# Performance work log

Hardware: AMD Instinct MI355X
Metric: run time of the kernel (lower is better)

Reference implementation:

```python
import jax, jax.numpy as jnp
import numpy as np

EPS = 1e-5
KEY_DIM = 32
V_DIM = 128  # att_ratio * key_dim
HEADS = 8


def bn2d(x, g, b):
    # BatchNorm2d, training-mode batch statistics: per-channel over (B, H, W)
    m = x.mean(axis=(0, 2, 3), keepdims=True)
    v = x.var(axis=(0, 2, 3), keepdims=True)
    xh = (x - m) * jax.lax.rsqrt(v + EPS)
    return xh * g[None, :, None, None] + b[None, :, None, None]


def conv1x1(x, w):
    # [B,Cin,H,W] x [Cout,Cin] -> [B,Cout,H,W]
    return jnp.einsum('bchw,oc->bohw', x, w)


def setup_inputs() -> dict:
    key = jax.random.key(0)
    ks = jax.random.split(key, 6)
    B, C, H, W = 8, 384, 32, 32
    s = 0.02
    return {
        'x': jax.random.normal(ks[0], (B, C, H, W), jnp.float32),
        'w_qkv': jax.random.normal(ks[1], (1536, 384), jnp.float32) * s,
        'g_qkv': jnp.ones((1536,), jnp.float32),
        'b_qkv': jnp.zeros((1536,), jnp.float32),
        'w_merge': jax.random.normal(ks[2], (384, 1024), jnp.float32) * s,
        'g_merge': jnp.ones((384,), jnp.float32),
        'b_merge': jnp.zeros((384,), jnp.float32),
        'w_fc1': jax.random.normal(ks[3], (768, 384), jnp.float32) * s,
        'g_fc1': jnp.ones((768,), jnp.float32),
        'b_fc1': jnp.zeros((768,), jnp.float32),
        'w_fc2': jax.random.normal(ks[4], (384, 768), jnp.float32) * s,
        'g_fc2': jnp.ones((384,), jnp.float32),
        'b_fc2': jnp.zeros((384,), jnp.float32),
    }


def reference(x, w_qkv, g_qkv, b_qkv, w_merge, g_merge, b_merge,
              w_fc1, g_fc1, b_fc1, w_fc2, g_fc2, b_fc2):
    B, C, H, W = x.shape
    N = H * W
    scale = KEY_DIM ** -0.5

    # ---- Attention block (conv path) ----
    qkv = bn2d(conv1x1(x, w_qkv), g_qkv, b_qkv)            # [B,1536,H,W]
    qkv = qkv.reshape(B, HEADS, KEY_DIM + KEY_DIM + V_DIM, N)
    q = qkv[:, :, :KEY_DIM]                                 # [B,h,dq,N]
    k = qkv[:, :, KEY_DIM:2 * KEY_DIM]                      # [B,h,dk,N]
    v = qkv[:, :, 2 * KEY_DIM:]                             # [B,h,dv,N]
    att = jnp.einsum('bhdn,bhdm->bhnm', q, k) * scale       # [B,h,N,N]
    att = jax.nn.softmax(att, axis=-1)
    o = jnp.einsum('bhnm,bhdm->bhdn', att, v)               # [B,h,dv,N]
    o = o.reshape(B, HEADS * V_DIM, H, W)                   # [B,1024,H,W]
    o = jax.nn.gelu(o, approximate=False)                   # merge.act
    o = bn2d(conv1x1(o, w_merge), g_merge, b_merge)         # [B,384,H,W]
    x = x + o                                               # residual

    # ---- ConvMlp block ----
    h = bn2d(conv1x1(x, w_fc1), g_fc1, b_fc1)               # [B,768,H,W]
    h = jax.nn.gelu(h, approximate=False)
    h = bn2d(conv1x1(h, w_fc2), g_fc2, b_fc2)               # [B,384,H,W]
    return x + h
```

## Files before the change

### kernel.cpp

```cpp
#include <hip/hip_runtime.h>
#include <hip/hip_bf16.h>
#include <math.h>


#define NPIX 1024
typedef __attribute__((ext_vector_type(8))) short short8;
typedef __attribute__((ext_vector_type(4))) float f32x4;
typedef unsigned long long ull;

__device__ __forceinline__ float gelu_exact(float v) {
    return 0.5f * v * (1.0f + erff(v * 0.70710678118654752f));
}
__device__ __forceinline__ short f2bf(float f) {
    unsigned u = __float_as_uint(f);
    unsigned r = (u + 0x7fffu + ((u >> 16) & 1u)) >> 16;
    return (short)r;
}
__device__ __forceinline__ ull pack4bf(float a, float b, float c, float d) {
    return  (ull)(unsigned short)f2bf(a)
         | ((ull)(unsigned short)f2bf(b) << 16)
         | ((ull)(unsigned short)f2bf(c) << 32)
         | ((ull)(unsigned short)f2bf(d) << 48);
}

__global__ __launch_bounds__(256) void cast4(
    const float* __restrict__ s0, const float* __restrict__ s1,
    const float* __restrict__ s2, const float* __restrict__ s3,
    short* __restrict__ d0, short* __restrict__ d1,
    short* __restrict__ d2, short* __restrict__ d3)
{
    int t = blockIdx.x * 256 + threadIdx.x;
    const float* s; short* d; int off;
    if (t < 73728)       { s = s0; d = d0; off = t; }
    else if (t < 122880) { s = s1; d = d1; off = t - 73728; }
    else if (t < 159744) { s = s2; d = d2; off = t - 122880; }
    else                 { s = s3; d = d3; off = t - 159744; }
    float4 a = *(const float4*)&s[(size_t)off * 8];
    float4 b = *(const float4*)&s[(size_t)off * 8 + 4];
    *(ull*)&d[(size_t)off * 8]     = pack4bf(a.x, a.y, a.z, a.w);
    *(ull*)&d[(size_t)off * 8 + 4] = pack4bf(b.x, b.y, b.z, b.w);
}

__global__ __launch_bounds__(256) void x_transpose(
    const float* __restrict__ x, short* __restrict__ x_bf, float* __restrict__ x_tf)
{
    __shared__ float ls[64][65];
    const int b = blockIdx.z, c0 = blockIdx.y * 64, n0 = blockIdx.x * 64;
    const int rl = threadIdx.x >> 6, ll = threadIdx.x & 63;
    #pragma unroll
    for (int it = 0; it < 16; ++it) {
        int c = rl + it * 4;
        ls[c][ll] = x[((size_t)b * 384 + c0 + c) * NPIX + n0 + ll];
    }
    __syncthreads();
    #pragma unroll
    for (int it = 0; it < 16; ++it) {
        int n = rl + it * 4;
        float v = ls[ll][n];
        size_t row = (size_t)b * NPIX + n0 + n;
        x_tf[row * 384 + c0 + ll] = v;
        x_bf[row * 384 + c0 + ll] = f2bf(v);
    }
}

__global__ __launch_bounds__(256) void gemm_bf16(
    const short* __restrict__ A, const short* __restrict__ Wt,
    float* __restrict__ D, float* __restrict__ sums, int O, int K)
{
    __shared__ short a_s[128 * 72];
    __shared__ short w_s[128 * 72];
    const int tid = threadIdx.x;
    const int wave = tid >> 6, lane = tid & 63;
    const int l16 = lane & 15, lhi = lane >> 4;
    const int m0 = blockIdx.x * 128, o0 = blockIdx.y * 128;
    const int wm = (wave & 1) * 64, wo = (wave >> 1) * 64;

    f32x4 acc[4][4];
    #pragma unroll
    for (int i = 0; i < 4; ++i)
        #pragma unroll
        for (int j = 0; j < 4; ++j) acc[i][j] = (f32x4){0.f, 0.f, 0.f, 0.f};

    for (int k0 = 0; k0 < K; k0 += 64) {
        #pragma unroll
        for (int it = 0; it < 4; ++it) {
            int idx = tid + it * 256;
            int r = idx >> 3, ch = idx & 7;
            *(float4*)&a_s[r * 72 + ch * 8] =
                *(const float4*)&A[(size_t)(m0 + r) * K + k0 + ch * 8];
            *(float4*)&w_s[r * 72 + ch * 8] =
                *(const float4*)&Wt[(size_t)(o0 + r) * K + k0 + ch * 8];
        }
        __syncthreads();
        #pragma unroll
        for (int kb = 0; kb < 2; ++kb) {
            short8 af[4], wf[4];
            #pragma unroll
            for (int i = 0; i < 4; ++i)
                af[i] = *(const short8*)&a_s[(wm + i * 16 + l16) * 72 + kb * 32 + lhi * 8];
            #pragma unroll
            for (int j = 0; j < 4; ++j)
                wf[j] = *(const short8*)&w_s[(wo + j * 16 + l16) * 72 + kb * 32 + lhi * 8];
            #pragma unroll
            for (int i = 0; i < 4; ++i)
                #pragma unroll
                for (int j = 0; j < 4; ++j)
                    acc[i][j] = __builtin_amdgcn_mfma_f32_16x16x32_bf16(af[i], wf[j], acc[i][j], 0, 0, 0);
        }
        __syncthreads();
    }

    #pragma unroll
    for (int i = 0; i < 4; ++i) {
        #pragma unroll
        for (int r = 0; r < 4; ++r) {
            size_t row = (size_t)(m0 + wm + i * 16 + lhi * 4 + r);
            #pragma unroll
            for (int j = 0; j < 4; ++j)
                D[row * O + o0 + wo + j * 16 + l16] = acc[i][j][r];
        }
    }
    #pragma unroll
    for (int j = 0; j < 4; ++j) {
        float s1 = 0.f, s2 = 0.f;
        #pragma unroll
        for (int i = 0; i < 4; ++i)
            #pragma unroll
            for (int r = 0; r < 4; ++r) { float v = acc[i][j][r]; s1 += v; s2 += v * v; }
        s1 += __shfl_xor(s1, 16); s1 += __shfl_xor(s1, 32);
        s2 += __shfl_xor(s2, 16); s2 += __shfl_xor(s2, 32);
        if (lhi == 0) {
            int col = o0 + wo + j * 16 + l16;
            atomicAdd(&sums[col * 2], s1);
            atomicAdd(&sums[col * 2 + 1], s2);
        }
    }
}

__global__ __launch_bounds__(256) void bn_finalize(
    const float* __restrict__ sums, const float* __restrict__ gamma,
    const float* __restrict__ beta, float* __restrict__ st, int O)
{
    int ch = blockIdx.x * 256 + threadIdx.x;
    if (ch >= O) return;
    float s = sums[ch * 2], ss = sums[ch * 2 + 1];
    float mean = s * (1.0f / 8192.0f);
    float var = ss * (1.0f / 8192.0f) - mean * mean;
    float sc = gamma[ch] * rsqrtf(var + 1e-5f);
    st[ch * 2] = sc;
    st[ch * 2 + 1] = beta[ch] - mean * sc;
}

__global__ __launch_bounds__(256) void qkv_post_vt(
    const float* __restrict__ raw, const float* __restrict__ st,
    short* __restrict__ qko, short* __restrict__ vto)
{
    __shared__ short ls[64][136];
    const int b = blockIdx.z, hp = blockIdx.y, n0 = blockIdx.x * 64;
    const int tid = threadIdx.x;
    const int r = tid >> 2, cg = tid & 3;
    const size_t rowbase = (size_t)(b * NPIX + n0 + r) * 1536;
    const float qs = 0.17677669529663687f * 1.4426950408889634f;

    {
        int hh = 2 * hp + (cg >> 1);
        int chb = hh * 192 + (cg & 1) * 32;
        bool isq = (cg & 1) == 0;
        size_t orow = (size_t)(b * NPIX + n0 + r) * 512 + hp * 128 + cg * 32;
        #pragma unroll
        for (int cc = 0; cc < 8; ++cc) {
            int ch = chb + cc * 4;
            float4 v  = *(const float4*)&raw[rowbase + ch];
            float4 sa = *(const float4*)&st[ch * 2];
            float4 sb = *(const float4*)&st[ch * 2 + 4];
            float o0 = v.x * sa.x + sa.y, o1 = v.y * sa.z + sa.w;
            float o2 = v.z * sb.x + sb.y, o3 = v.w * sb.z + sb.w;
            if (isq) { o0 *= qs; o1 *= qs; o2 *= qs; o3 *= qs; }
            *(ull*)&qko[orow + cc * 4] = pack4bf(o0, o1, o2, o3);
        }
    }
    #pragma unroll
    for (int hv = 0; hv < 2; ++hv) {
        int h = 2 * hp + hv;
        __syncthreads();
        #pragma unroll
        for (int cc = 0; cc < 8; ++cc) {
            int ch = h * 192 + 64 + cg * 32 + cc * 4;
            float4 v  = *(const float4*)&raw[rowbase + ch];
            float4 sa = *(const float4*)&st[ch * 2];
            float4 sb = *(const float4*)&st[ch * 2 + 4];
            float o0 = v.x * sa.x + sa.y, o1 = v.y * sa.z + sa.w;
            float o2 = v.z * sb.x + sb.y, o3 = v.w * sb.z + sb.w;
            *(ull*)&ls[r][cg * 32 + cc * 4] = pack4bf(o0, o1, o2, o3);
        }
        __syncthreads();
        int dv = tid >> 1, nh = tid & 1;
        size_t obase = ((size_t)(b * 8 + h) * 128 + dv) * NPIX + n0 + nh * 32;
        #pragma unroll
        for (int j = 0; j < 8; ++j) {
            int n = nh * 32 + j * 4;
            ull u =  (ull)(unsigned short)ls[n][dv]
                  | ((ull)(unsigned short)ls[n + 1][dv] << 16)
                  | ((ull)(unsigned short)ls[n + 2][dv] << 32)
                  | ((ull)(unsigned short)ls[n + 3][dv] << 48);
            *(ull*)&vto[obase + j * 4] = u;
        }
    }
}

#define ATTN_TILE(M0, KCUR, KNEXT)                                            \
{                                                                             \
    const int m0_ = (M0);                                                     \
    f32x4 s0_[4], s1_[4];                                                     \
    _Pragma("unroll")                                                         \
    for (int fm = 0; fm < 4; ++fm) {                                          \
        s0_[fm] = (f32x4){0.f, 0.f, 0.f, 0.f};                                \
        s1_[fm] = (f32x4){0.f, 0.f, 0.f, 0.f};                                \
    }                                                                         \
    _Pragma("unroll")                                                         \
    for (int fm = 0; fm < 4; ++fm) {                                          \
        s0_[fm] = __builtin_amdgcn_mfma_f32_16x16x32_bf16(KCUR[fm], qf0, s0_[fm], 0, 0, 0); \
        s1_[fm] = __builtin_amdgcn_mfma_f32_16x16x32_bf16(KCUR[fm], qf1, s1_[fm], 0, 0, 0); \
    }                                                                         \
    short8 vf_[16];                                                           \
    _Pragma("unroll")                                                         \
    for (int kc = 0; kc < 2; ++kc)                                            \
        _Pragma("unroll")                                                     \
        for (int fdv = 0; fdv < 8; ++fdv)                                     \
            vf_[kc * 8 + fdv] = *(const short8*)&vb[(size_t)(fdv * 16 + l16) * NPIX + m0_ + kc * 32 + lhi * 8]; \
    {                                                                         \
        int mn_ = (m0_ + 64) & 1023;                                          \
        _Pragma("unroll")                                                     \
        for (int fm = 0; fm < 4; ++fm)                                        \
            KNEXT[fm] = *(const short8*)&kb[(size_t)(mn_ + fm * 16 + l16) * 512 + lhi * 8]; \
    }                                                                         \
    float mx0 = fmaxf(fmaxf(s0_[0][0], s0_[0][1]), fmaxf(s0_[0][2], s0_[0][3])); \
    float mx1 = fmaxf(fmaxf(s1_[0][0], s1_[0][1]), fmaxf(s1_[0][2], s1_[0][3])); \
    _Pragma("unroll")                                                         \
    for (int fm = 1; fm < 4; ++fm) {                                          \
        mx0 = fmaxf(mx0, fmaxf(fmaxf(s0_[fm][0], s0_[fm][1]), fmaxf(s0_[fm][2], s0_[fm][3]))); \
        mx1 = fmaxf(mx1, fmaxf(fmaxf(s1_[fm][0], s1_[fm][1]), fmaxf(s1_[fm][2], s1_[fm][3]))); \
    }                                                                         \
    mx0 = fmaxf(mx0, __shfl_xor(mx0, 16)); mx0 = fmaxf(mx0, __shfl_xor(mx0, 32)); \
    mx1 = fmaxf(mx1, __shfl_xor(mx1, 16)); mx1 = fmaxf(mx1, __shfl_xor(mx1, 32)); \
    bool need_ = (mx0 > m_run0 + 11.0f) || (mx1 > m_run1 + 11.0f);            \
    if (__any(need_)) {                                                       \
        float mn0 = fmaxf(m_run0, mx0), f0 = exp2f(m_run0 - mn0);             \
        float mn1 = fmaxf(m_run1, mx1), f1 = exp2f(m_run1 - mn1);             \
        m_run0 = mn0; m_run1 = mn1; l_run0 *= f0; l_run1 *= f1;               \
        _Pragma("unroll")                                                     \
        for (int rr = 0; rr < 4; ++rr) {                                      \
            float fb0 = __shfl(f0, lhi * 4 + rr);                             \
            float fb1 = __shfl(f1, lhi * 4 + rr);                             \
            _Pragma("unroll")                                                 \
            for (int fdv = 0; fdv < 8; ++fdv) {                               \
                acc[0][fdv][rr] *= fb0;                                       \
                acc[1][fdv][rr] *= fb1;                                       \
            }                                                                 \
        }                                                                     \
    }                                                                         \
    float rs0 = 0.f, rs1 = 0.f;                                               \
    _Pragma("unroll")                                                         \
    for (int fm = 0; fm < 4; ++fm) {                                          \
        float p0 = exp2f(s0_[fm][0] - m_run0), p1 = exp2f(s0_[fm][1] - m_run0); \
        float p2 = exp2f(s0_[fm][2] - m_run0), p3 = exp2f(s0_[fm][3] - m_run0); \
        rs0 += (p0 + p1) + (p2 + p3);                                         \
        *(ull*)&pw[l16 * 72 + fm * 16 + lhi * 4] = pack4bf(p0, p1, p2, p3);   \
        float t0 = exp2f(s1_[fm][0] - m_run1), t1 = exp2f(s1_[fm][1] - m_run1); \
        float t2 = exp2f(s1_[fm][2] - m_run1), t3 = exp2f(s1_[fm][3] - m_run1); \
        rs1 += (t0 + t1) + (t2 + t3);                                         \
        *(ull*)&pw[(16 + l16) * 72 + fm * 16 + lhi * 4] = pack4bf(t0, t1, t2, t3); \
    }                                                                         \
    rs0 += __shfl_xor(rs0, 16); rs0 += __shfl_xor(rs0, 32);                   \
    rs1 += __shfl_xor(rs1, 16); rs1 += __shfl_xor(rs1, 32);                   \
    l_run0 += rs0; l_run1 += rs1;                                             \
    asm volatile("s_waitcnt lgkmcnt(0)" ::: "memory");                        \
    _Pragma("unroll")                                                         \
    for (int kc = 0; kc < 2; ++kc) {                                          \
        short8 pf0 = *(const short8*)&pw[l16 * 72 + kc * 32 + lhi * 8];       \
        short8 pf1 = *(const short8*)&pw[(16 + l16) * 72 + kc * 32 + lhi * 8]; \
        _Pragma("unroll")                                                     \
        for (int fdv = 0; fdv < 8; ++fdv) {                                   \
            acc[0][fdv] = __builtin_amdgcn_mfma_f32_16x16x32_bf16(pf0, vf_[kc * 8 + fdv], acc[0][fdv], 0, 0, 0); \
            acc[1][fdv] = __builtin_amdgcn_mfma_f32_16x16x32_bf16(pf1, vf_[kc * 8 + fdv], acc[1][fdv], 0, 0, 0); \
        }                                                                     \
    }                                                                         \
}

__global__ __launch_bounds__(64) void attn_kernel(
    const short* __restrict__ qk, const short* __restrict__ vt, short* __restrict__ outp)
{
    __shared__ short pw[32 * 72];
    const int id0 = blockIdx.x;
    const int swz = (id0 & 7) * 256 + (id0 >> 3);
    const int qt = swz & 31, bh = swz >> 5;
    const int h = bh & 7, b = bh >> 3;
    const int q0 = qt * 32;
    const int lane = threadIdx.x;
    const int l16 = lane & 15, lhi = lane >> 4;

    const short* qkb = qk + (size_t)b * NPIX * 512 + h * 64;
    const short* kb  = qkb + 32;
    const short* vb  = vt + (size_t)bh * 128 * NPIX;

    short8 qf0 = *(const short8*)&qkb[(size_t)(q0 + l16) * 512 + lhi * 8];
    short8 qf1 = *(const short8*)&qkb[(size_t)(q0 + 16 + l16) * 512 + lhi * 8];

    f32x4 acc[2][8];
    #pragma unroll
    for (int i = 0; i < 2; ++i)
        #pragma unroll
        for (int j = 0; j < 8; ++j) acc[i][j] = (f32x4){0.f, 0.f, 0.f, 0.f};
    float m_run0 = -1e30f, m_run1 = -1e30f, l_run0 = 0.f, l_run1 = 0.f;

    short8 kfA[4], kfB[4];
    #pragma unroll
    for (int fm = 0; fm < 4; ++fm)
        kfA[fm] = *(const short8*)&kb[(size_t)(fm * 16 + l16) * 512 + lhi * 8];

    for (int mt = 0; mt < 16; mt += 2) {
        ATTN_TILE(mt * 64,      kfA, kfB)
        ATTN_TILE(mt * 64 + 64, kfB, kfA)
    }

    #pragma unroll
    for (int rr = 0; rr < 4; ++rr) {
        float inv0 = 1.0f / __shfl(l_run0, lhi * 4 + rr);
        float inv1 = 1.0f / __shfl(l_run1, lhi * 4 + rr);
        size_t row0 = (size_t)b * NPIX + q0 + lhi * 4 + rr;
        #pragma unroll
        for (int fdv = 0; fdv < 8; ++fdv) {
            float o0 = acc[0][fdv][rr] * inv0;
            float o1 = acc[1][fdv][rr] * inv1;
            outp[row0 * 1024 + h * 128 + fdv * 16 + l16] = f2bf(gelu_exact(o0));
            outp[(row0 + 16) * 1024 + h * 128 + fdv * 16 + l16] = f2bf(gelu_exact(o1));
        }
    }
}

__global__ __launch_bounds__(256) void x2_kernel(
    const float* __restrict__ raw, const float* __restrict__ st,
    const float* __restrict__ xtf, float* __restrict__ x2f, short* __restrict__ x2bf)
{
    int t = blockIdx.x * 256 + threadIdx.x;
    int row = t / 96, c = (t % 96) * 4;
    size_t idx = (size_t)row * 384 + c;
    float4 v  = *(const float4*)&raw[idx];
    float4 xr = *(const float4*)&xtf[idx];
    float4 sa = *(const float4*)&st[c * 2];
    float4 sb = *(const float4*)&st[c * 2 + 4];
    float o0 = xr.x + v.x * sa.x + sa.y;
    float o1 = xr.y + v.y * sa.z + sa.w;
    float o2 = xr.z + v.z * sb.x + sb.y;
    float o3 = xr.w + v.w * sb.z + sb.w;
    *(float4*)&x2f[idx] = make_float4(o0, o1, o2, o3);
    *(ull*)&x2bf[idx] = pack4bf(o0, o1, o2, o3);
}

__global__ __launch_bounds__(256) void h_kernel(
    const float* __restrict__ raw, const float* __restrict__ st, short* __restrict__ hbf)
{
    int t = blockIdx.x * 256 + threadIdx.x;
    int row = t / 192, c = (t % 192) * 4;
    size_t idx = (size_t)row * 768 + c;
    float4 v  = *(const float4*)&raw[idx];
    float4 sa = *(const float4*)&st[c * 2];
    float4 sb = *(const float4*)&st[c * 2 + 4];
    float o0 = gelu_exact(v.x * sa.x + sa.y);
    float o1 = gelu_exact(v.y * sa.z + sa.w);
    float o2 = gelu_exact(v.z * sb.x + sb.y);
    float o3 = gelu_exact(v.w * sb.z + sb.w);
    *(ull*)&hbf[idx] = pack4bf(o0, o1, o2, o3);
}

__global__ __launch_bounds__(256) void final_tr(
    const float* __restrict__ raw, const float* __restrict__ st,
    const float* __restrict__ x2f, float* __restrict__ out)
{
    __shared__ float ls[64][65];
    const int b = blockIdx.z, c0 = blockIdx.y * 64, n0 = blockIdx.x * 64;
    const int rl = threadIdx.x >> 6, ll = threadIdx.x & 63;
    const int c = c0 + ll;
    const float sc = st[c * 2], sh = st[c * 2 + 1];
    #pragma unroll
    for (int it = 0; it < 16; ++it) {
        int n = rl + it * 4;
        size_t idx = ((size_t)b * NPIX + n0 + n) * 384 + c;
        ls[n][ll] = x2f[idx] + raw[idx] * sc + sh;
    }
    __syncthreads();
    #pragma unroll
    for (int it = 0; it < 16; ++it) {
        int cr = rl + it * 4;
        out[((size_t)b * 384 + c0 + cr) * NPIX + n0 + ll] = ls[ll][cr];
    }
}

extern "C" void kernel_launch(void* const* d_in, const int* in_sizes, int n_in,
                              void* d_out, int out_size, void* d_ws, size_t ws_size,
                              hipStream_t stream)
{
    const float* x       = (const float*)d_in[0];
    const float* w_qkv   = (const float*)d_in[1];
    const float* g_qkv   = (const float*)d_in[2];
    const float* b_qkv   = (const float*)d_in[3];
    const float* w_merge = (const float*)d_in[4];
    const float* g_merge = (const float*)d_in[5];
    const float* b_merge = (const float*)d_in[6];
    const float* w_fc1   = (const float*)d_in[7];
    const float* g_fc1   = (const float*)d_in[8];
    const float* b_fc1   = (const float*)d_in[9];
    const float* w_fc2   = (const float*)d_in[10];
    const float* g_fc2   = (const float*)d_in[11];
    const float* b_fc2   = (const float*)d_in[12];
    float* out = (float*)d_out;

    char* ws = (char*)d_ws;
    short* wq_bf   = (short*)(ws + 0);
    short* wm_bf   = (short*)(ws + 1179648);
    short* wf1_bf  = (short*)(ws + 1966080);
    short* wf2_bf  = (short*)(ws + 2555904);
    short* x_bf    = (short*)(ws + 3145728);
    float* x_tf    = (float*)(ws + 9437184);
    float* qkv_raw = (float*)(ws + 22020096);
    short* qk_bf   = (short*)(ws + 72351744);
    short* vt      = (short*)(ws + 80740352);
    short* attn_bf = (short*)(ws + 22020096);
    float* fc1_raw = (float*)(ws + 38797312);
    float* fc2_raw = (float*)(ws + 22020096);
    short* h_bf    = (short*)(ws + 80740352);
    float* merge_raw = (float*)(ws + 97517568);
    short* x2_bf   = (short*)(ws + 110100480);
    float* x2_f    = (float*)(ws + 116391936);
    float* sums    = (float*)(ws + 128974848);
    float* stats   = (float*)(ws + 128999424);

    float* sums_qkv = sums;
    float* sums_mg  = sums + 1536 * 2;
    float* sums_f1  = sums + (1536 + 384) * 2;
    float* sums_f2  = sums + (1536 + 384 + 768) * 2;
    float* st_qkv = stats;
    float* st_mg  = stats + 1536 * 2;
    float* st_f1  = stats + (1536 + 384) * 2;
    float* st_f2  = stats + (1536 + 384 + 768) * 2;

    hipMemsetAsync(sums, 0, 3072 * 2 * sizeof(float), stream);

    cast4<<<768, 256, 0, stream>>>(w_qkv, w_merge, w_fc1, w_fc2,
                                   wq_bf, wm_bf, wf1_bf, wf2_bf);
    x_transpose<<<dim3(16, 6, 8), 256, 0, stream>>>(x, x_bf, x_tf);

    gemm_bf16<<<dim3(64, 12), 256, 0, stream>>>(x_bf, wq_bf, qkv_raw, sums_qkv, 1536, 384);
    bn_finalize<<<6, 256, 0, stream>>>(sums_qkv, g_qkv, b_qkv, st_qkv, 1536);
    qkv_post_vt<<<dim3(16, 4, 8), 256, 0, stream>>>(qkv_raw, st_qkv, qk_bf, vt);

    attn_kernel<<<2048, 64, 0, stream>>>(qk_bf, vt, attn_bf);

    gemm_bf16<<<dim3(64, 3), 256, 0, stream>>>(attn_bf, wm_bf, merge_raw, sums_mg, 384, 1024);
    bn_finalize<<<2, 256, 0, stream>>>(sums_mg, g_merge, b_merge, st_mg, 384);
    x2_kernel<<<3072, 256, 0, stream>>>(merge_raw, st_mg, x_tf, x2_f, x2_bf);

    gemm_bf16<<<dim3(64, 6), 256, 0, stream>>>(x2_bf, wf1_bf, fc1_raw, sums_f1, 768, 384);
    bn_finalize<<<3, 256, 0, stream>>>(sums_f1, g_fc1, b_fc1, st_f1, 768);
    h_kernel<<<6144, 256, 0, stream>>>(fc1_raw, sums_f1 == sums_f1 ? st_f1 : st_f1, h_bf);

    gemm_bf16<<<dim3(64, 3), 256, 0, stream>>>(h_bf, wf2_bf, fc2_raw, sums_f2, 384, 768);
    bn_finalize<<<2, 256, 0, stream>>>(sums_f2, g_fc2, b_fc2, st_f2, 384);
    final_tr<<<dim3(16, 6, 8), 256, 0, stream>>>(fc2_raw, st_f2, x2_f, out);
}
```

Baseline: 342.8 us.

## Fuse BN finalize into GEMMs, emit bf16 outputs, and repack QKV into fragment layout

Merges the weight cast, the x transpose and the stats zeroing into one prep kernel. Each GEMM now computes its BatchNorm scale and shift in the last-finishing block, using an atomic counter, so the separate finalize launches go away. The QKV, merge and fc1 GEMMs store bf16 instead of fp32, cutting intermediate memory traffic. A new repack kernel lays Q, K and V out in MFMA-fragment-linear order with the Q and K BN folded into Q; the V BN moves into the attention epilogue. The cost is extra bf16 rounding before normalization and reliance on a threadfence plus atomic-counter last-block pattern.

After: 441.7 us. 28.8% more time.

```diff
diff --git a/kernel.cpp b/kernel.cpp
--- a/kernel.cpp
+++ b/kernel.cpp
@@ -15,6 +15,9 @@
     unsigned u = __float_as_uint(f);
     unsigned r = (u + 0x7fffu + ((u >> 16) & 1u)) >> 16;
     return (short)r;
+}
+__device__ __forceinline__ float bf2f(short s) {
+    return __uint_as_float(((unsigned)(unsigned short)s) << 16);
 }
 __device__ __forceinline__ ull pack4bf(float a, float b, float c, float d) {
     return  (ull)(unsigned short)f2bf(a)
@@ -23,49 +26,60 @@
          | ((ull)(unsigned short)f2bf(d) << 48);
 }
 
-__global__ __launch_bounds__(256) void cast4(
+__global__ __launch_bounds__(256) void prep_kernel(
+    const float* __restrict__ x,
     const float* __restrict__ s0, const float* __restrict__ s1,
     const float* __restrict__ s2, const float* __restrict__ s3,
     short* __restrict__ d0, short* __restrict__ d1,
-    short* __restrict__ d2, short* __restrict__ d3)
-{
-    int t = blockIdx.x * 256 + threadIdx.x;
-    const float* s; short* d; int off;
-    if (t < 73728)       { s = s0; d = d0; off = t; }
-    else if (t < 122880) { s = s1; d = d1; off = t - 73728; }
-    else if (t < 159744) { s = s2; d = d2; off = t - 122880; }
-    else                 { s = s3; d = d3; off = t - 159744; }
-    float4 a = *(const float4*)&s[(size_t)off * 8];
-    float4 b = *(const float4*)&s[(size_t)off * 8 + 4];
-    *(ull*)&d[(size_t)off * 8]     = pack4bf(a.x, a.y, a.z, a.w);
-    *(ull*)&d[(size_t)off * 8 + 4] = pack4bf(b.x, b.y, b.z, b.w);
-}
-
-__global__ __launch_bounds__(256) void x_transpose(
-    const float* __restrict__ x, short* __restrict__ x_bf, float* __restrict__ x_tf)
-{
-    __shared__ float ls[64][65];
-    const int b = blockIdx.z, c0 = blockIdx.y * 64, n0 = blockIdx.x * 64;
-    const int rl = threadIdx.x >> 6, ll = threadIdx.x & 63;
-    #pragma unroll
-    for (int it = 0; it < 16; ++it) {
-        int c = rl + it * 4;
-        ls[c][ll] = x[((size_t)b * 384 + c0 + c) * NPIX + n0 + ll];
-    }
-    __syncthreads();
-    #pragma unroll
-    for (int it = 0; it < 16; ++it) {
-        int n = rl + it * 4;
-        float v = ls[ll][n];
-        size_t row = (size_t)b * NPIX + n0 + n;
-        x_tf[row * 384 + c0 + ll] = v;
-        x_bf[row * 384 + c0 + ll] = f2bf(v);
-    }
-}
-
+    short* __restrict__ d2, short* __restrict__ d3,
+    short* __restrict__ x_bf, float* __restrict__ x_tf,
+    float* __restrict__ sums, int* __restrict__ cnt)
+{
+    const int bid = blockIdx.x, tid = threadIdx.x;
+    if (bid < 768) {
+        __shared__ float ls[64][65];
+        const int n0 = (bid & 15) * 64;
+        const int cy = (bid >> 4) % 6, b = (bid >> 4) / 6;
+        const int c0 = cy * 64;
+        const int rl = tid >> 6, ll = tid & 63;
+        #pragma unroll
+        for (int it = 0; it < 16; ++it) {
+            int c = rl + it * 4;
+            ls[c][ll] = x[((size_t)b * 384 + c0 + c) * NPIX + n0 + ll];
+        }
+        __syncthreads();
+        #pragma unroll
+        for (int it = 0; it < 16; ++it) {
+            int n = rl + it * 4;
+            float v = ls[ll][n];
+            size_t row = (size_t)b * NPIX + n0 + n;
+            x_tf[row * 384 + c0 + ll] = v;
+            x_bf[row * 384 + c0 + ll] = f2bf(v);
+        }
+    } else if (bid < 1536) {
+        int t = (bid - 768) * 256 + tid;
+        const float* s; short* d; int off;
+        if (t < 73728)       { s = s0; d = d0; off = t; }
+        else if (t < 122880) { s = s1; d = d1; off = t - 73728; }
+        else if (t < 159744) { s = s2; d = d2; off = t - 122880; }
+        else                 { s = s3; d = d3; off = t - 159744; }
+        float4 a = *(const float4*)&s[(size_t)off * 8];
+        float4 b = *(const float4*)&s[(size_t)off * 8 + 4];
+        *(ull*)&d[(size_t)off * 8]     = pack4bf(a.x, a.y, a.z, a.w);
+        *(ull*)&d[(size_t)off * 8 + 4] = pack4bf(b.x, b.y, b.z, b.w);
+    } else {
+        for (int i = tid; i < 6144; i += 256) sums[i] = 0.f;
+        if (tid < 4) cnt[tid] = 0;
+    }
+}
+
+template<typename OT>
 __global__ __launch_bounds__(256) void gemm_bf16(
     const short* __restrict__ A, const short* __restrict__ Wt,
-    float* __restrict__ D, float* __restrict__ sums, int O, int K)
+    OT* __restrict__ D, float* __restrict__ sums,
+    const float* __restrict__ gamma, const float* __restrict__ beta,
+    float* __restrict__ st, int* __restrict__ cnt,
+    int O, int K, int nblk)
 {
     __shared__ short a_s[128 * 72];
     __shared__ short w_s[128 * 72];
@@ -116,8 +130,12 @@
         for (int r = 0; r < 4; ++r) {
             size_t row = (size_t)(m0 + wm + i * 16 + lhi * 4 + r);
             #pragma unroll
-            for (int j = 0; j < 4; ++j)
-                D[row * O + o0 + wo + j * 16 + l16] = acc[i][j][r];
+            for (int j = 0; j < 4; ++j) {
+                if constexpr (sizeof(OT) == 2)
+                    D[row * O + o0 + wo + j * 16 + l16] = f2bf(acc[i][j][r]);
+                else
+                    D[row * O + o0 + wo + j * 16 + l16] = acc[i][j][r];
+            }
         }
     }
     #pragma unroll
@@ -135,82 +153,101 @@
             atomicAdd(&sums[col * 2 + 1], s2);
         }
     }
-}
-
-__global__ __launch_bounds__(256) void bn_finalize(
-    const float* __restrict__ sums, const float* __restrict__ gamma,
-    const float* __restrict__ beta, float* __restrict__ st, int O)
-{
-    int ch = blockIdx.x * 256 + threadIdx.x;
-    if (ch >= O) return;
-    float s = sums[ch * 2], ss = sums[ch * 2 + 1];
-    float mean = s * (1.0f / 8192.0f);
-    float var = ss * (1.0f / 8192.0f) - mean * mean;
-    float sc = gamma[ch] * rsqrtf(var + 1e-5f);
-    st[ch * 2] = sc;
-    st[ch * 2 + 1] = beta[ch] - mean * sc;
-}
-
-__global__ __launch_bounds__(256) void qkv_post_vt(
-    const float* __restrict__ raw, const float* __restrict__ st,
-    short* __restrict__ qko, short* __restrict__ vto)
-{
-    __shared__ short ls[64][136];
-    const int b = blockIdx.z, hp = blockIdx.y, n0 = blockIdx.x * 64;
-    const int tid = threadIdx.x;
-    const int r = tid >> 2, cg = tid & 3;
-    const size_t rowbase = (size_t)(b * NPIX + n0 + r) * 1536;
-    const float qs = 0.17677669529663687f * 1.4426950408889634f;
+    __threadfence();
+    __syncthreads();
+    __shared__ int lastf;
+    if (tid == 0) lastf = (atomicAdd(cnt, 1) == nblk - 1) ? 1 : 0;
+    __syncthreads();
+    if (lastf) {
+        __threadfence();
+        for (int ch = tid; ch < O; ch += 256) {
+            float s  = atomicAdd(&sums[ch * 2], 0.0f);
+            float ss = atomicAdd(&sums[ch * 2 + 1], 0.0f);
+            float mean = s * (1.0f / 8192.0f);
+            float var  = ss * (1.0f / 8192.0f) - mean * mean;
+            float sc = gamma[ch] * rsqrtf(var + 1e-5f);
+            st[ch * 2] = sc;
+            st[ch * 2 + 1] = beta[ch] - mean * sc;
+        }
+    }
+}
+
+__global__ __launch_bounds__(256) void repack_qkv(
+    const short* __restrict__ qkvbf, const float* __restrict__ st,
+    short* __restrict__ qlin, short* __restrict__ klin, short* __restrict__ vlin)
+{
+    __shared__ short ls[64][130];
+    const int mt = blockIdx.x, bh = blockIdx.y;
+    const int b = bh >> 3, h = bh & 7;
+    const int chb = h * 192;
+    const int n0 = mt * 64;
+    const int t = threadIdx.x;
+    const int n = t >> 2, lhi = t & 3, l16 = n & 15;
+    const size_t rowb = (size_t)(b * NPIX + n0 + n) * 1536;
 
     {
-        int hh = 2 * hp + (cg >> 1);
-        int chb = hh * 192 + (cg & 1) * 32;
-        bool isq = (cg & 1) == 0;
-        size_t orow = (size_t)(b * NPIX + n0 + r) * 512 + hp * 128 + cg * 32;
-        #pragma unroll
-        for (int cc = 0; cc < 8; ++cc) {
-            int ch = chb + cc * 4;
-            float4 v  = *(const float4*)&raw[rowbase + ch];
-            float4 sa = *(const float4*)&st[ch * 2];
-            float4 sb = *(const float4*)&st[ch * 2 + 4];
-            float o0 = v.x * sa.x + sa.y, o1 = v.y * sa.z + sa.w;
-            float o2 = v.z * sb.x + sb.y, o3 = v.w * sb.z + sb.w;
-            if (isq) { o0 *= qs; o1 *= qs; o2 *= qs; o3 *= qs; }
-            *(ull*)&qko[orow + cc * 4] = pack4bf(o0, o1, o2, o3);
-        }
-    }
-    #pragma unroll
-    for (int hv = 0; hv < 2; ++hv) {
-        int h = 2 * hp + hv;
-        __syncthreads();
-        #pragma unroll
-        for (int cc = 0; cc < 8; ++cc) {
-            int ch = h * 192 + 64 + cg * 32 + cc * 4;
-            float4 v  = *(const float4*)&raw[rowbase + ch];
-            float4 sa = *(const float4*)&st[ch * 2];
-            float4 sb = *(const float4*)&st[ch * 2 + 4];
-            float o0 = v.x * sa.x + sa.y, o1 = v.y * sa.z + sa.w;
-            float o2 = v.z * sb.x + sb.y, o3 = v.w * sb.z + sb.w;
-            *(ull*)&ls[r][cg * 32 + cc * 4] = pack4bf(o0, o1, o2, o3);
-        }
-        __syncthreads();
-        int dv = tid >> 1, nh = tid & 1;
-        size_t obase = ((size_t)(b * 8 + h) * 128 + dv) * NPIX + n0 + nh * 32;
-        #pragma unroll
-        for (int j = 0; j < 8; ++j) {
-            int n = nh * 32 + j * 4;
-            ull u =  (ull)(unsigned short)ls[n][dv]
-                  | ((ull)(unsigned short)ls[n + 1][dv] << 16)
-                  | ((ull)(unsigned short)ls[n + 2][dv] << 32)
-                  | ((ull)(unsigned short)ls[n + 3][dv] << 48);
-            *(ull*)&vto[obase + j * 4] = u;
-        }
-    }
-}
-
-#define ATTN_TILE(M0, KCUR, KNEXT)                                            \
+        const float S = 0.17677669529663687f * 1.4426950408889634f;
+        int cq = chb + lhi * 8;
+        short8 qr = *(const short8*)&qkvbf[rowb + cq];
+        float4 a0 = *(const float4*)&st[cq * 2];
+        float4 a1 = *(const float4*)&st[cq * 2 + 4];
+        float4 a2 = *(const float4*)&st[cq * 2 + 8];
+        float4 a3 = *(const float4*)&st[cq * 2 + 12];
+        float4 k0 = *(const float4*)&st[(cq + 32) * 2];
+        float4 k1 = *(const float4*)&st[(cq + 32) * 2 + 4];
+        float4 k2 = *(const float4*)&st[(cq + 32) * 2 + 8];
+        float4 k3 = *(const float4*)&st[(cq + 32) * 2 + 12];
+        float q0 = (bf2f(qr[0]) * a0.x + a0.y) * k0.x * S;
+        float q1 = (bf2f(qr[1]) * a0.z + a0.w) * k0.z * S;
+        float q2 = (bf2f(qr[2]) * a1.x + a1.y) * k1.x * S;
+        float q3 = (bf2f(qr[3]) * a1.z + a1.w) * k1.z * S;
+        float q4 = (bf2f(qr[4]) * a2.x + a2.y) * k2.x * S;
+        float q5 = (bf2f(qr[5]) * a2.z + a2.w) * k2.z * S;
+        float q6 = (bf2f(qr[6]) * a3.x + a3.y) * k3.x * S;
+        float q7 = (bf2f(qr[7]) * a3.z + a3.w) * k3.z * S;
+        int fq = (n >> 4) & 1, qtl = n >> 5;
+        size_t qo = (size_t)bh * 32768 +
+                    ((((size_t)mt * 2 + qtl) * 2 + fq) * 64 + lhi * 16 + l16) * 8;
+        *(ull*)&qlin[qo]     = pack4bf(q0, q1, q2, q3);
+        *(ull*)&qlin[qo + 4] = pack4bf(q4, q5, q6, q7);
+    }
+    {
+        short8 kr = *(const short8*)&qkvbf[rowb + chb + 32 + lhi * 8];
+        int fm = n >> 4;
+        size_t ko = (size_t)bh * 32768 +
+                    (((size_t)mt * 4 + fm) * 64 + lhi * 16 + l16) * 8;
+        *(short8*)&klin[ko] = kr;
+    }
+    #pragma unroll
+    for (int i = 0; i < 4; ++i) {
+        short8 v8 = *(const short8*)&qkvbf[rowb + chb + 64 + lhi * 32 + i * 8];
+        *(short8*)&ls[n][lhi * 32 + i * 8] = v8;
+    }
+    __syncthreads();
+    #pragma unroll
+    for (int u = 0; u < 4; ++u) {
+        int unit = t + u * 256;
+        int kc = unit >> 9, fdv = (unit >> 6) & 7, lane = unit & 63;
+        int lh = lane >> 4, l1 = lane & 15;
+        int col = fdv * 16 + l1;
+        int rbase = kc * 32 + lh * 8;
+        short v8[8];
+        #pragma unroll
+        for (int e = 0; e < 8; ++e) v8[e] = ls[rbase + e][col];
+        size_t vo = (size_t)bh * 131072 +
+                    (((size_t)mt * 2 + kc) * 8 + fdv) * 512 + (size_t)lane * 8;
+        ull u0 =  (ull)(unsigned short)v8[0] | ((ull)(unsigned short)v8[1] << 16)
+               | ((ull)(unsigned short)v8[2] << 32) | ((ull)(unsigned short)v8[3] << 48);
+        ull u1 =  (ull)(unsigned short)v8[4] | ((ull)(unsigned short)v8[5] << 16)
+               | ((ull)(unsigned short)v8[6] << 32) | ((ull)(unsigned short)v8[7] << 48);
+        *(ull*)&vlin[vo]     = u0;
+        *(ull*)&vlin[vo + 4] = u1;
+    }
+}
+
+#define ATTN_TILE(TT, KCUR, KNEXT)                                            \
 {                                                                             \
-    const int m0_ = (M0);                                                     \
+    const int tt_ = (TT);                                                     \
     f32x4 s0_[4], s1_[4];                                                     \
     _Pragma("unroll")                                                         \
     for (int fm = 0; fm < 4; ++fm) {                                          \
@@ -227,12 +264,12 @@
     for (int kc = 0; kc < 2; ++kc)                                            \
         _Pragma("unroll")                                                     \
         for (int fdv = 0; fdv < 8; ++fdv)                                     \
-            vf_[kc * 8 + fdv] = *(const short8*)&vb[(size_t)(fdv * 16 + l16) * NPIX + m0_ + kc * 32 + lhi * 8]; \
+            vf_[kc * 8 + fdv] = *(const short8*)&vb[((((size_t)tt_ * 2 + kc) * 8 + fdv) * 64 + lane) * 8]; \
     {                                                                         \
-        int mn_ = (m0_ + 64) & 1023;                                          \
+        int tn_ = (tt_ + 1) & 15;                                             \
         _Pragma("unroll")                                                     \
         for (int fm = 0; fm < 4; ++fm)                                        \
-            KNEXT[fm] = *(const short8*)&kb[(size_t)(mn_ + fm * 16 + l16) * 512 + lhi * 8]; \
+            KNEXT[fm] = *(const short8*)&kb[((((size_t)tn_ * 4 + fm) * 64) + lane) * 8]; \
     }                                                                         \
     float mx0 = fmaxf(fmaxf(s0_[0][0], s0_[0][1]), fmaxf(s0_[0][2], s0_[0][3])); \
     float mx1 = fmaxf(fmaxf(s1_[0][0], s1_[0][1]), fmaxf(s1_[0][2], s1_[0][3])); \
@@ -288,7 +325,9 @@
 }
 
 __global__ __launch_bounds__(64) void attn_kernel(
-    const short* __restrict__ qk, const short* __restrict__ vt, short* __restrict__ outp)
+    const short* __restrict__ qlin, const short* __restrict__ klin,
+    const short* __restrict__ vlin, const float* __restrict__ st,
+    short* __restrict__ outp)
 {
     __shared__ short pw[32 * 72];
     const int id0 = blockIdx.x;
@@ -299,12 +338,12 @@
     const int lane = threadIdx.x;
     const int l16 = lane & 15, lhi = lane >> 4;
 
-    const short* qkb = qk + (size_t)b * NPIX * 512 + h * 64;
-    const short* kb  = qkb + 32;
-    const short* vb  = vt + (size_t)bh * 128 * NPIX;
-
-    short8 qf0 = *(const short8*)&qkb[(size_t)(q0 + l16) * 512 + lhi * 8];
-    short8 qf1 = *(const short8*)&qkb[(size_t)(q0 + 16 + l16) * 512 + lhi * 8];
+    const short* qb = qlin + (size_t)bh * 32768;
+    const short* kb = klin + (size_t)bh * 32768;
+    const short* vb = vlin + (size_t)bh * 131072;
+
+    short8 qf0 = *(const short8*)&qb[(((size_t)qt * 2 + 0) * 64 + lane) * 8];
+    short8 qf1 = *(const short8*)&qb[(((size_t)qt * 2 + 1) * 64 + lane) * 8];
 
     f32x4 acc[2][8];
     #pragma unroll
@@ -316,13 +355,19 @@
     short8 kfA[4], kfB[4];
     #pragma unroll
     for (int fm = 0; fm < 4; ++fm)
-        kfA[fm] = *(const short8*)&kb[(size_t)(fm * 16 + l16) * 512 + lhi * 8];
+        kfA[fm] = *(const short8*)&kb[((size_t)fm * 64 + lane) * 8];
 
     for (int mt = 0; mt < 16; mt += 2) {
-        ATTN_TILE(mt * 64,      kfA, kfB)
-        ATTN_TILE(mt * 64 + 64, kfB, kfA)
-    }
-
+        ATTN_TILE(mt,     kfA, kfB)
+        ATTN_TILE(mt + 1, kfB, kfA)
+    }
+
+    float scv[8], shv[8];
+    #pragma unroll
+    for (int fdv = 0; fdv < 8; ++fdv) {
+        int cv = h * 192 + 64 + fdv * 16 + l16;
+        scv[fdv] = st[cv * 2]; shv[fdv] = st[cv * 2 + 1];
+    }
     #pragma unroll
     for (int rr = 0; rr < 4; ++rr) {
         float inv0 = 1.0f / __shfl(l_run0, lhi * 4 + rr);
@@ -330,8 +375,8 @@
         size_t row0 = (size_t)b * NPIX + q0 + lhi * 4 + rr;
         #pragma unroll
         for (int fdv = 0; fdv < 8; ++fdv) {
-            float o0 = acc[0][fdv][rr] * inv0;
-            float o1 = acc[1][fdv][rr] * inv1;
+            float o0 = acc[0][fdv][rr] * inv0 * scv[fdv] + shv[fdv];
+            float o1 = acc[1][fdv][rr] * inv1 * scv[fdv] + shv[fdv];
             outp[row0 * 1024 + h * 128 + fdv * 16 + l16] = f2bf(gelu_exact(o0));
             outp[(row0 + 16) * 1024 + h * 128 + fdv * 16 + l16] = f2bf(gelu_exact(o1));
         }
@@ -339,38 +384,40 @@
 }
 
 __global__ __launch_bounds__(256) void x2_kernel(
-    const float* __restrict__ raw, const float* __restrict__ st,
+    const short* __restrict__ raw, const float* __restrict__ st,
     const float* __restrict__ xtf, float* __restrict__ x2f, short* __restrict__ x2bf)
 {
     int t = blockIdx.x * 256 + threadIdx.x;
-    int row = t / 96, c = (t % 96) * 4;
+    int row = t / 48, c = (t % 48) * 8;
     size_t idx = (size_t)row * 384 + c;
-    float4 v  = *(const float4*)&raw[idx];
-    float4 xr = *(const float4*)&xtf[idx];
-    float4 sa = *(const float4*)&st[c * 2];
-    float4 sb = *(const float4*)&st[c * 2 + 4];
-    float o0 = xr.x + v.x * sa.x + sa.y;
-    float o1 = xr.y + v.y * sa.z + sa.w;
-    float o2 = xr.z + v.z * sb.x + sb.y;
-    float o3 = xr.w + v.w * sb.z + sb.w;
-    *(float4*)&x2f[idx] = make_float4(o0, o1, o2, o3);
-    *(ull*)&x2bf[idx] = pack4bf(o0, o1, o2, o3);
+    short8 v8 = *(const short8*)&raw[idx];
+    float o[8];
+    #pragma unroll
+    for (int j = 0; j < 8; ++j) {
+        float sc = st[(c + j) * 2], sh = st[(c + j) * 2 + 1];
+        o[j] = xtf[idx + j] + bf2f(v8[j]) * sc + sh;
+    }
+    *(float4*)&x2f[idx]     = make_float4(o[0], o[1], o[2], o[3]);
+    *(float4*)&x2f[idx + 4] = make_float4(o[4], o[5], o[6], o[7]);
+    *(ull*)&x2bf[idx]     = pack4bf(o[0], o[1], o[2], o[3]);
+    *(ull*)&x2bf[idx + 4] = pack4bf(o[4], o[5], o[6], o[7]);
 }
 
 __global__ __launch_bounds__(256) void h_kernel(
-    const float* __restrict__ raw, const float* __restrict__ st, short* __restrict__ hbf)
+    const short* __restrict__ raw, const float* __restrict__ st, short* __restrict__ hbf)
 {
     int t = blockIdx.x * 256 + threadIdx.x;
-    int row = t / 192, c = (t % 192) * 4;
+    int row = t / 96, c = (t % 96) * 8;
     size_t idx = (size_t)row * 768 + c;
-    float4 v  = *(const float4*)&raw[idx];
-    float4 sa = *(const float4*)&st[c * 2];
-    float4 sb = *(const float4*)&st[c * 2 + 4];
-    float o0 = gelu_exact(v.x * sa.x + sa.y);
-    float o1 = gelu_exact(v.y * sa.z + sa.w);
-    float o2 = gelu_exact(v.z * sb.x + sb.y);
-    float o3 = gelu_exact(v.w * sb.z + sb.w);
-    *(ull*)&hbf[idx] = pack4bf(o0, o1, o2, o3);
+    short8 v8 = *(const short8*)&raw[idx];
+    float o[8];
+    #pragma unroll
+    for (int j = 0; j < 8; ++j) {
+        float sc = st[(c + j) * 2], sh = st[(c + j) * 2 + 1];
+        o[j] = gelu_exact(bf2f(v8[j]) * sc + sh);
+    }
+    *(ull*)&hbf[idx]     = pack4bf(o[0], o[1], o[2], o[3]);
+    *(ull*)&hbf[idx + 4] = pack4bf(o[4], o[5], o[6], o[7]);
 }
 
 __global__ __launch_bounds__(256) void final_tr(
@@ -422,18 +469,20 @@
     short* wf2_bf  = (short*)(ws + 2555904);
     short* x_bf    = (short*)(ws + 3145728);
     float* x_tf    = (float*)(ws + 9437184);
-    float* qkv_raw = (float*)(ws + 22020096);
-    short* qk_bf   = (short*)(ws + 72351744);
-    short* vt      = (short*)(ws + 80740352);
+    short* qkv_bf  = (short*)(ws + 22020096);
     short* attn_bf = (short*)(ws + 22020096);
-    float* fc1_raw = (float*)(ws + 38797312);
     float* fc2_raw = (float*)(ws + 22020096);
-    short* h_bf    = (short*)(ws + 80740352);
-    float* merge_raw = (float*)(ws + 97517568);
-    short* x2_bf   = (short*)(ws + 110100480);
-    float* x2_f    = (float*)(ws + 116391936);
-    float* sums    = (float*)(ws + 128974848);
-    float* stats   = (float*)(ws + 128999424);
+    short* q_lin   = (short*)(ws + 47185920);
+    short* merge_bf= (short*)(ws + 47185920);
+    short* k_lin   = (short*)(ws + 51380224);
+    short* v_lin   = (short*)(ws + 55574528);
+    float* x2_f    = (float*)(ws + 55574528);
+    short* x2_bf   = (short*)(ws + 72351744);
+    short* fc1_bf  = (short*)(ws + 78643200);
+    short* h_bf    = (short*)(ws + 91226112);
+    float* sums    = (float*)(ws + 103809024);
+    float* stats   = (float*)(ws + 103833600);
+    int*   cnt     = (int*)  (ws + 103858176);
 
     float* sums_qkv = sums;
     float* sums_mg  = sums + 1536 * 2;
@@ -444,27 +493,29 @@
     float* st_f1  = stats + (1536 + 384) * 2;
     float* st_f2  = stats + (1536 + 384 + 768) * 2;
 
-    hipMemsetAsync(sums, 0, 3072 * 2 * sizeof(float), stream);
-
-    cast4<<<768, 256, 0, stream>>>(w_qkv, w_merge, w_fc1, w_fc2,
-                                   wq_bf, wm_bf, wf1_bf, wf2_bf);
-    x_transpose<<<dim3(16, 6, 8), 256, 0, stream>>>(x, x_bf, x_tf);
-
-    gemm_bf16<<<dim3(64, 12), 256, 0, stream>>>(x_bf, wq_bf, qkv_raw, sums_qkv, 1536, 384);
-    bn_finalize<<<6, 256, 0, stream>>>(sums_qkv, g_qkv, b_qkv, st_qkv, 1536);
-    qkv_post_vt<<<dim3(16, 4, 8), 256, 0, stream>>>(qkv_raw, st_qkv, qk_bf, vt);
-
-    attn_kernel<<<2048, 64, 0, stream>>>(qk_bf, vt, attn_bf);
-
-    gemm_bf16<<<dim3(64, 3), 256, 0, stream>>>(attn_bf, wm_bf, merge_raw, sums_mg, 384, 1024);
-    bn_finalize<<<2, 256, 0, stream>>>(sums_mg, g_merge, b_merge, st_mg, 384);
-    x2_kernel<<<3072, 256, 0, stream>>>(merge_raw, st_mg, x_tf, x2_f, x2_bf);
-
-    gemm_bf16<<<dim3(64, 6), 256, 0, stream>>>(x2_bf, wf1_bf, fc1_raw, sums_f1, 768, 384);
-    bn_finalize<<<3, 256, 0, stream>>>(sums_f1, g_fc1, b_fc1, st_f1, 768);
-    h_kernel<<<6144, 256, 0, stream>>>(fc1_raw, sums_f1 == sums_f1 ? st_f1 : st_f1, h_bf);
-
-    gemm_bf16<<<dim3(64, 3), 256, 0, stream>>>(h_bf, wf2_bf, fc2_raw, sums_f2, 384, 768);
-    bn_finalize<<<2, 256, 0, stream>>>(sums_f2, g_fc2, b_fc2, st_f2, 384);
+    prep_kernel<<<1537, 256, 0, stream>>>(x, w_qkv, w_merge, w_fc1, w_fc2,
+                                          wq_bf, wm_bf, wf1_bf, wf2_bf,
+                                          x_bf, x_tf, sums, cnt);
+
+    gemm_bf16<short><<<dim3(64, 12), 256, 0, stream>>>(
+        x_bf, wq_bf, qkv_bf, sums_qkv, g_qkv, b_qkv, st_qkv, cnt + 0, 1536, 384, 768);
+
+    repack_qkv<<<dim3(16, 64), 256, 0, stream>>>(qkv_bf, st_qkv, q_lin, k_lin, v_lin);
+
+    attn_kernel<<<2048, 64, 0, stream>>>(q_lin, k_lin, v_lin, st_qkv, attn_bf);
+
+    gemm_bf16<short><<<dim3(64, 3), 256, 0, stream>>>(
+        attn_bf, wm_bf, merge_bf, sums_mg, g_merge, b_merge, st_mg, cnt + 1, 384, 1024, 192);
+
+    x2_kernel<<<1536, 256, 0, stream>>>(merge_bf, st_mg, x_tf, x2_f, x2_bf);
+
+    gemm_bf16<short><<<dim3(64, 6), 256, 0, stream>>>(
+        x2_bf, wf1_bf, fc1_bf, sums_f1, g_fc1, b_fc1, st_f1, cnt + 2, 768, 384, 384);
+
+    h_kernel<<<3072, 256, 0, stream>>>(fc1_bf, st_f1, h_bf);
+
+    gemm_bf16<float><<<dim3(64, 3), 256, 0, stream>>>(
+        h_bf, wf2_bf, fc2_raw, sums_f2, g_fc2, b_fc2, st_f2, cnt + 3, 384, 768, 192);
+
     final_tr<<<dim3(16, 6, 8), 256, 0, stream>>>(fc2_raw, st_f2, x2_f, out);
 }
```
